# Optimization experiments

Hardware: AMD Instinct MI355X
Metric: run time of the kernel (lower is better)

Reference implementation:

```python
import jax, jax.numpy as jnp
import numpy as np

EMBED = 512
QDIM = 512
VDIM = 512
SRC = 4096
BSZ = 64


def setup_inputs() -> dict:
    key = jax.random.key(0)
    ks = jax.random.split(key, 6)
    query = jax.random.normal(ks[0], (BSZ, QDIM), dtype=jnp.float32)
    value = jax.random.normal(ks[1], (SRC, BSZ, VDIM), dtype=jnp.float32)
    key_padding_mask = jnp.zeros((SRC, BSZ), dtype=bool)
    # params: torch init uniform(-0.1, 0.1); b=0, g=sqrt(1/embed)
    Wq = jax.random.uniform(ks[2], (EMBED, QDIM), minval=-0.1, maxval=0.1, dtype=jnp.float32)
    Wv = jax.random.uniform(ks[3], (EMBED, VDIM), minval=-0.1, maxval=0.1, dtype=jnp.float32)
    v = jax.random.uniform(ks[4], (EMBED,), minval=-0.1, maxval=0.1, dtype=jnp.float32)
    b = jnp.zeros((EMBED,), dtype=jnp.float32)
    g = jnp.full((1,), np.sqrt(1.0 / EMBED), dtype=jnp.float32)
    return {"query": query, "value": value, "key_padding_mask": key_padding_mask,
            "Wq": Wq, "Wv": Wv, "v": v, "b": b, "g": g}


def reference(query, value, key_padding_mask, Wq, Wv, v, b, g):
    # projected_query: [1, bsz, embed]; key: [src, bsz, embed]
    pq = (query @ Wq.T)[None, :, :]
    key = jnp.einsum('sbv,ev->sbe', value, Wv)
    normed_v = g * v / jnp.linalg.norm(v)  # [embed]
    # attn_scores: [src, bsz]
    attn_scores = jnp.einsum('e,sbe->sb', normed_v, jnp.tanh(pq + key + b))
    attn_scores = jnp.where(key_padding_mask, -jnp.inf, attn_scores)
    attn_scores = jax.nn.softmax(attn_scores, axis=0)
    # context: [bsz, value_dim]
    context = jnp.einsum('sb,sbv->bv', attn_scores, value)
    return (context, attn_scores, attn_scores)
```

## Files before the change

kernel.cpp:

```cpp
#include <hip/hip_runtime.h>
#include <hip/hip_bf16.h>
#include <math.h>

typedef __bf16 bf16x8 __attribute__((ext_vector_type(8)));
typedef __bf16 bf16x4 __attribute__((ext_vector_type(4)));
typedef float  f32x4  __attribute__((ext_vector_type(4)));

#define SRC 4096
#define BSZ 64
#define EMB 512
#define LDA 520

__device__ __forceinline__ float fast_tanh(float x) {
  float ax = fabsf(x);
  float t  = __expf(-2.0f * ax);
  float r  = 1.0f - 2.0f * t / (1.0f + t);
  return copysignf(r, x);
}

__global__ void prep_nv(const float* __restrict__ v, const float* __restrict__ g,
                        float* __restrict__ nv) {
  __shared__ float red[256];
  int t = threadIdx.x;
  float a = v[t], b = v[t + 256];
  red[t] = a * a + b * b;
  __syncthreads();
  for (int o = 128; o > 0; o >>= 1) {
    if (t < o) red[t] += red[t + o];
    __syncthreads();
  }
  float scale = g[0] / sqrtf(red[0]);
  nv[t]       = a * scale;
  nv[t + 256] = b * scale;
}

__global__ void prep_pqb(const float* __restrict__ query, const float* __restrict__ Wq,
                         const float* __restrict__ bias, float* __restrict__ pqb) {
  __shared__ float q[EMB];
  int b = blockIdx.x, t = threadIdx.x;
  q[t]       = query[b * EMB + t];
  q[t + 256] = query[b * EMB + t + 256];
  __syncthreads();
  for (int e = t; e < EMB; e += 256) {
    const float* wr = Wq + (size_t)e * EMB;
    float acc = 0.f;
#pragma unroll 4
    for (int k = 0; k < EMB; k += 4) {
      float4 qv = *reinterpret_cast<const float4*>(&q[k]);
      float4 wv = *reinterpret_cast<const float4*>(&wr[k]);
      acc += qv.x * wv.x + qv.y * wv.y + qv.z * wv.z + qv.w * wv.w;
    }
    pqb[b * EMB + e] = acc + bias[e];
  }
}

__global__ void pack_wv(const float* __restrict__ Wv, __bf16* __restrict__ wvpk) {
  int tid  = blockIdx.x * 256 + threadIdx.x;
  int lane = tid & 63;
  int ks   = (tid >> 6) & 15;
  int nsub = tid >> 10;
  int e  = nsub * 16 + (lane & 15);
  int k0 = ks * 32 + (lane >> 4) * 8;
  const float* src = Wv + (size_t)e * EMB + k0;
  bf16x8 o;
#pragma unroll
  for (int j = 0; j < 8; ++j) o[j] = (__bf16)src[j];
  *reinterpret_cast<bf16x8*>(wvpk + (size_t)tid * 8) = o;
}

__global__ __launch_bounds__(256, 2)
void scores_kernel(const float* __restrict__ value, const float* __restrict__ pqb,
                   const float* __restrict__ nv, const __bf16* __restrict__ wvpk,
                   float* __restrict__ scoresT) {
  __shared__ __bf16 As[BSZ * LDA];
  __shared__ float red[4][BSZ];
  const int s = blockIdx.x;
  const int t = threadIdx.x;

  const float* src = value + (size_t)s * (BSZ * EMB);
#pragma unroll
  for (int i = 0; i < 32; ++i) {
    int e0 = (i * 256 + t) * 4;
    float4 vv = *reinterpret_cast<const float4*>(src + e0);
    int row = e0 >> 9;
    int col = e0 & 511;
    bf16x4 o;
    o[0] = (__bf16)vv.x; o[1] = (__bf16)vv.y; o[2] = (__bf16)vv.z; o[3] = (__bf16)vv.w;
    *reinterpret_cast<bf16x4*>(&As[row * LDA + col]) = o;
  }
  __syncthreads();

  const int w  = t >> 6;
  const int l  = t & 63;
  const int lr = l & 15;
  const int lk = l >> 4;

  float sc[16];
#pragma unroll
  for (int i = 0; i < 16; ++i) sc[i] = 0.f;

  for (int outer = 0; outer < 2; ++outer) {
    const int nbase = outer * 256 + w * 64;
    f32x4 acc[4][4];
#pragma unroll
    for (int m = 0; m < 4; ++m)
#pragma unroll
      for (int n = 0; n < 4; ++n)
#pragma unroll
        for (int r = 0; r < 4; ++r) acc[m][n][r] = 0.f;

#pragma unroll 2
    for (int ks = 0; ks < 16; ++ks) {
      bf16x8 a[4], bfr[4];
#pragma unroll
      for (int m = 0; m < 4; ++m)
        a[m] = *reinterpret_cast<const bf16x8*>(&As[(m * 16 + lr) * LDA + ks * 32 + lk * 8]);
#pragma unroll
      for (int n = 0; n < 4; ++n)
        bfr[n] = *reinterpret_cast<const bf16x8*>(
            wvpk + ((size_t)((((nbase >> 4) + n) * 16 + ks) * 64 + l)) * 8);
#pragma unroll
      for (int m = 0; m < 4; ++m)
#pragma unroll
        for (int n = 0; n < 4; ++n)
          acc[m][n] = __builtin_amdgcn_mfma_f32_16x16x32_bf16(a[m], bfr[n], acc[m][n], 0, 0, 0);
    }

#pragma unroll
    for (int n = 0; n < 4; ++n) {
      int col = nbase + n * 16 + lr;
      float nvc = nv[col];
#pragma unroll
      for (int m = 0; m < 4; ++m) {
#pragma unroll
        for (int r = 0; r < 4; ++r) {
          int brow = m * 16 + lk * 4 + r;
          float x = acc[m][n][r] + pqb[brow * EMB + col];
          sc[m * 4 + r] += nvc * fast_tanh(x);
        }
      }
    }
  }

#pragma unroll
  for (int i = 0; i < 16; ++i) {
    float vsum = sc[i];
#pragma unroll
    for (int off = 1; off < 16; off <<= 1) vsum += __shfl_xor(vsum, off, 64);
    if (lr == 0) red[w][(i >> 2) * 16 + lk * 4 + (i & 3)] = vsum;
  }
  __syncthreads();
  if (t < BSZ) {
    float total = red[0][t] + red[1][t] + red[2][t] + red[3][t];
    scoresT[(size_t)t * SRC + s] = total;
  }
}

__global__ void softmax_k(const float* __restrict__ scoresT, const unsigned char* __restrict__ mask,
                          float* __restrict__ pT, float* __restrict__ attn0,
                          float* __restrict__ attn1) {
  __shared__ float buf[SRC];
  __shared__ float red[256];
  int b = blockIdx.x, t = threadIdx.x;
  float mx = -1e30f;
  for (int s = t; s < SRC; s += 256) {
    float x = scoresT[(size_t)b * SRC + s];
    if (mask[(size_t)s * BSZ + b]) x = -1e30f;
    buf[s] = x;
    mx = fmaxf(mx, x);
  }
  red[t] = mx; __syncthreads();
  for (int o = 128; o > 0; o >>= 1) { if (t < o) red[t] = fmaxf(red[t], red[t + o]); __syncthreads(); }
  mx = red[0]; __syncthreads();
  float sum = 0.f;
  for (int s = t; s < SRC; s += 256) { float e = __expf(buf[s] - mx); buf[s] = e; sum += e; }
  red[t] = sum; __syncthreads();
  for (int o = 128; o > 0; o >>= 1) { if (t < o) red[t] += red[t + o]; __syncthreads(); }
  float inv = 1.0f / red[0];
  for (int s = t; s < SRC; s += 256) {
    float p = buf[s] * inv;
    pT[(size_t)b * SRC + s] = p;
    attn0[(size_t)s * BSZ + b] = p;
    attn1[(size_t)s * BSZ + b] = p;
  }
}

__global__ void ctx_partial(const float* __restrict__ value, const float* __restrict__ pT,
                            float* __restrict__ parts) {
  int blk = blockIdx.x;
  int c = blk >> 6;
  int b = blk & 63;
  int t = threadIdx.x;
  float2 acc = make_float2(0.f, 0.f);
#pragma unroll 4
  for (int i = 0; i < 128; ++i) {
    int s = c * 128 + i;
    float p = pT[(size_t)b * SRC + s];
    float2 vv = *reinterpret_cast<const float2*>(value + ((size_t)(s * BSZ + b)) * EMB + t * 2);
    acc.x += p * vv.x;
    acc.y += p * vv.y;
  }
  *reinterpret_cast<float2*>(parts + (size_t)blk * EMB + t * 2) = acc;
}

__global__ void ctx_reduce(const float* __restrict__ parts, float* __restrict__ out_ctx) {
  int idx = blockIdx.x * 256 + threadIdx.x;
  float acc = 0.f;
#pragma unroll
  for (int c = 0; c < 32; ++c) acc += parts[(size_t)c * (BSZ * EMB) + idx];
  out_ctx[idx] = acc;
}

extern "C" void kernel_launch(void* const* d_in, const int* in_sizes, int n_in,
                              void* d_out, int out_size, void* d_ws, size_t ws_size,
                              hipStream_t stream) {
  const float* query        = (const float*)d_in[0];
  const float* value        = (const float*)d_in[1];
  const unsigned char* mask = (const unsigned char*)d_in[2];
  const float* Wq           = (const float*)d_in[3];
  const float* Wv           = (const float*)d_in[4];
  const float* v            = (const float*)d_in[5];
  const float* bias         = (const float*)d_in[6];
  const float* g            = (const float*)d_in[7];

  float* out_ctx = (float*)d_out;
  float* attn0   = (float*)d_out + BSZ * EMB;
  float* attn1   = attn0 + SRC * BSZ;

  char* ws = (char*)d_ws;
  float*  nv      = (float*)(ws);
  float*  pqb     = (float*)(ws + 2048);
  __bf16* wvpk    = (__bf16*)(ws + 2048 + 131072);
  float*  scoresT = (float*)(ws + 2048 + 131072 + 524288);
  float*  pT      = scoresT + SRC * BSZ;
  float*  parts   = pT + SRC * BSZ;

  prep_nv<<<1, 256, 0, stream>>>(v, g, nv);
  prep_pqb<<<BSZ, 256, 0, stream>>>(query, Wq, bias, pqb);
  pack_wv<<<128, 256, 0, stream>>>(Wv, wvpk);
  scores_kernel<<<SRC, 256, 0, stream>>>(value, pqb, nv, wvpk, scoresT);
  softmax_k<<<BSZ, 256, 0, stream>>>(scoresT, mask, pT, attn0, attn1);
  ctx_partial<<<BSZ * 32, 256, 0, stream>>>(value, pT, parts);
  ctx_reduce<<<128, 256, 0, stream>>>(parts, out_ctx);
}
```

Before: 1.043 ms.

## Pipeline value staging in scores kernel with swizzled LDS and wider blocks

The scores kernel now runs 512 threads per block, one 64-column tile per warp, and stages value in four 128-wide K chunks. Each chunk is loaded into registers while the previous chunks feed MFMAs, through a double-buffered, XOR-swizzled LDS layout that replaces the padded full-row copy. This is meant to hide global load latency and cut LDS use so more blocks fit per CU, at the cost of extra barriers. Separately, prep_pqb is split across twice as many blocks with two accumulators, and ctx_partial switches to float4 loads with 128 threads.

```diff
diff --git a/kernel.cpp b/kernel.cpp
--- a/kernel.cpp
+++ b/kernel.cpp
@@ -9,7 +9,6 @@
 #define SRC 4096
 #define BSZ 64
 #define EMB 512
-#define LDA 520
 
 __device__ __forceinline__ float fast_tanh(float x) {
   float ax = fabsf(x);
@@ -37,21 +36,23 @@
 __global__ void prep_pqb(const float* __restrict__ query, const float* __restrict__ Wq,
                          const float* __restrict__ bias, float* __restrict__ pqb) {
   __shared__ float q[EMB];
-  int b = blockIdx.x, t = threadIdx.x;
+  int b = blockIdx.x >> 1, t = threadIdx.x;
+  int e = (blockIdx.x & 1) * 256 + t;
   q[t]       = query[b * EMB + t];
   q[t + 256] = query[b * EMB + t + 256];
   __syncthreads();
-  for (int e = t; e < EMB; e += 256) {
-    const float* wr = Wq + (size_t)e * EMB;
-    float acc = 0.f;
-#pragma unroll 4
-    for (int k = 0; k < EMB; k += 4) {
-      float4 qv = *reinterpret_cast<const float4*>(&q[k]);
-      float4 wv = *reinterpret_cast<const float4*>(&wr[k]);
-      acc += qv.x * wv.x + qv.y * wv.y + qv.z * wv.z + qv.w * wv.w;
-    }
-    pqb[b * EMB + e] = acc + bias[e];
-  }
+  const float* wr = Wq + (size_t)e * EMB;
+  float a0 = 0.f, a1 = 0.f;
+#pragma unroll 8
+  for (int k = 0; k < EMB; k += 8) {
+    float4 q0 = *reinterpret_cast<const float4*>(&q[k]);
+    float4 w0 = *reinterpret_cast<const float4*>(&wr[k]);
+    float4 q1 = *reinterpret_cast<const float4*>(&q[k + 4]);
+    float4 w1 = *reinterpret_cast<const float4*>(&wr[k + 4]);
+    a0 += q0.x * w0.x + q0.y * w0.y + q0.z * w0.z + q0.w * w0.w;
+    a1 += q1.x * w1.x + q1.y * w1.y + q1.z * w1.z + q1.w * w1.w;
+  }
+  pqb[b * EMB + e] = a0 + a1 + bias[e];
 }
 
 __global__ void pack_wv(const float* __restrict__ Wv, __bf16* __restrict__ wvpk) {
@@ -68,80 +69,104 @@
   *reinterpret_cast<bf16x8*>(wvpk + (size_t)tid * 8) = o;
 }
 
-__global__ __launch_bounds__(256, 2)
+__global__ __launch_bounds__(512, 4)
 void scores_kernel(const float* __restrict__ value, const float* __restrict__ pqb,
                    const float* __restrict__ nv, const __bf16* __restrict__ wvpk,
                    float* __restrict__ scoresT) {
-  __shared__ __bf16 As[BSZ * LDA];
-  __shared__ float red[4][BSZ];
+  __shared__ __bf16 As[2][64 * 128];
+  __shared__ float red[8][BSZ];
   const int s = blockIdx.x;
   const int t = threadIdx.x;
-
-  const float* src = value + (size_t)s * (BSZ * EMB);
-#pragma unroll
-  for (int i = 0; i < 32; ++i) {
-    int e0 = (i * 256 + t) * 4;
-    float4 vv = *reinterpret_cast<const float4*>(src + e0);
-    int row = e0 >> 9;
-    int col = e0 & 511;
-    bf16x4 o;
-    o[0] = (__bf16)vv.x; o[1] = (__bf16)vv.y; o[2] = (__bf16)vv.z; o[3] = (__bf16)vv.w;
-    *reinterpret_cast<bf16x4*>(&As[row * LDA + col]) = o;
-  }
-  __syncthreads();
-
   const int w  = t >> 6;
   const int l  = t & 63;
   const int lr = l & 15;
   const int lk = l >> 4;
 
-  float sc[16];
-#pragma unroll
-  for (int i = 0; i < 16; ++i) sc[i] = 0.f;
-
-  for (int outer = 0; outer < 2; ++outer) {
-    const int nbase = outer * 256 + w * 64;
-    f32x4 acc[4][4];
-#pragma unroll
-    for (int m = 0; m < 4; ++m)
-#pragma unroll
-      for (int n = 0; n < 4; ++n)
-#pragma unroll
-        for (int r = 0; r < 4; ++r) acc[m][n][r] = 0.f;
-
-#pragma unroll 2
-    for (int ks = 0; ks < 16; ++ks) {
-      bf16x8 a[4], bfr[4];
-#pragma unroll
-      for (int m = 0; m < 4; ++m)
-        a[m] = *reinterpret_cast<const bf16x8*>(&As[(m * 16 + lr) * LDA + ks * 32 + lk * 8]);
-#pragma unroll
-      for (int n = 0; n < 4; ++n)
-        bfr[n] = *reinterpret_cast<const bf16x8*>(
-            wvpk + ((size_t)((((nbase >> 4) + n) * 16 + ks) * 64 + l)) * 8);
-#pragma unroll
-      for (int m = 0; m < 4; ++m)
+  const int srow = t >> 3;
+  const int ssub = t & 7;
+  const float* sbase = value + (size_t)s * (BSZ * EMB) + (size_t)srow * EMB + ssub * 4;
+
+  float4 h0[4], h1[4];
+  auto issue = [&](int c, float4* h) {
+    const float* p = sbase + c * 128;
+#pragma unroll
+    for (int j = 0; j < 4; ++j) h[j] = *reinterpret_cast<const float4*>(p + j * 32);
+  };
+  auto write_lds = [&](int buf, const float4* h) {
+#pragma unroll
+    for (int j = 0; j < 4; ++j) {
+      int kg  = (ssub >> 1) + j * 4;
+      int kgp = kg ^ (srow & 7);
+      bf16x4 o;
+      o[0] = (__bf16)h[j].x; o[1] = (__bf16)h[j].y;
+      o[2] = (__bf16)h[j].z; o[3] = (__bf16)h[j].w;
+      *reinterpret_cast<bf16x4*>(&As[buf][srow * 128 + kgp * 8 + (ssub & 1) * 4]) = o;
+    }
+  };
+
+  f32x4 acc[4][4];
+#pragma unroll
+  for (int m = 0; m < 4; ++m)
+#pragma unroll
+    for (int n = 0; n < 4; ++n)
+#pragma unroll
+      for (int r = 0; r < 4; ++r) acc[m][n][r] = 0.f;
+
+  auto compute_chunk = [&](int buf, int c) {
+#pragma unroll
+    for (int ks = 0; ks < 4; ++ks) {
+      const int ksg = c * 4 + ks;
+      bf16x8 bq[4];
+#pragma unroll
+      for (int n = 0; n < 4; ++n) {
+        int nt = w * 4 + n;
+        bq[n] = *reinterpret_cast<const bf16x8*>(
+            wvpk + ((size_t)((nt * 16 + ksg) * 64 + l)) * 8);
+      }
+      const int kgp = ((ks * 4 + lk) ^ (lr & 7)) * 8;
+#pragma unroll
+      for (int m = 0; m < 4; ++m) {
+        bf16x8 a = *reinterpret_cast<const bf16x8*>(&As[buf][(m * 16 + lr) * 128 + kgp]);
 #pragma unroll
         for (int n = 0; n < 4; ++n)
-          acc[m][n] = __builtin_amdgcn_mfma_f32_16x16x32_bf16(a[m], bfr[n], acc[m][n], 0, 0, 0);
-    }
-
-#pragma unroll
-    for (int n = 0; n < 4; ++n) {
-      int col = nbase + n * 16 + lr;
-      float nvc = nv[col];
-#pragma unroll
-      for (int m = 0; m < 4; ++m) {
-#pragma unroll
-        for (int r = 0; r < 4; ++r) {
-          int brow = m * 16 + lk * 4 + r;
-          float x = acc[m][n][r] + pqb[brow * EMB + col];
-          sc[m * 4 + r] += nvc * fast_tanh(x);
-        }
+          acc[m][n] = __builtin_amdgcn_mfma_f32_16x16x32_bf16(a, bq[n], acc[m][n], 0, 0, 0);
       }
     }
-  }
-
+  };
+
+  issue(0, h0);
+  issue(1, h1);
+  write_lds(0, h0);
+  write_lds(1, h1);
+  __syncthreads();
+  issue(2, h0);
+  issue(3, h1);
+  compute_chunk(0, 0);
+  compute_chunk(1, 1);
+  __syncthreads();
+  write_lds(0, h0);
+  write_lds(1, h1);
+  __syncthreads();
+  compute_chunk(0, 2);
+  compute_chunk(1, 3);
+
+  float sc[16];
+#pragma unroll
+  for (int i = 0; i < 16; ++i) sc[i] = 0.f;
+#pragma unroll
+  for (int n = 0; n < 4; ++n) {
+    int col = w * 64 + n * 16 + lr;
+    float nvc = nv[col];
+#pragma unroll
+    for (int m = 0; m < 4; ++m) {
+#pragma unroll
+      for (int r = 0; r < 4; ++r) {
+        int brow = m * 16 + lk * 4 + r;
+        float x = acc[m][n][r] + pqb[brow * EMB + col];
+        sc[m * 4 + r] += nvc * fast_tanh(x);
+      }
+    }
+  }
 #pragma unroll
   for (int i = 0; i < 16; ++i) {
     float vsum = sc[i];
@@ -151,7 +176,9 @@
   }
   __syncthreads();
   if (t < BSZ) {
-    float total = red[0][t] + red[1][t] + red[2][t] + red[3][t];
+    float total = 0.f;
+#pragma unroll
+    for (int ww = 0; ww < 8; ++ww) total += red[ww][t];
     scoresT[(size_t)t * SRC + s] = total;
   }
 }
@@ -191,16 +218,16 @@
   int c = blk >> 6;
   int b = blk & 63;
   int t = threadIdx.x;
-  float2 acc = make_float2(0.f, 0.f);
-#pragma unroll 4
+  const float* pb = pT + (size_t)b * SRC + c * 128;
+  float4 acc = make_float4(0.f, 0.f, 0.f, 0.f);
+#pragma unroll 8
   for (int i = 0; i < 128; ++i) {
-    int s = c * 128 + i;
-    float p = pT[(size_t)b * SRC + s];
-    float2 vv = *reinterpret_cast<const float2*>(value + ((size_t)(s * BSZ + b)) * EMB + t * 2);
-    acc.x += p * vv.x;
-    acc.y += p * vv.y;
-  }
-  *reinterpret_cast<float2*>(parts + (size_t)blk * EMB + t * 2) = acc;
+    float p = pb[i];
+    float4 vv = *reinterpret_cast<const float4*>(
+        value + ((size_t)((c * 128 + i) * BSZ + b)) * EMB + t * 4);
+    acc.x += p * vv.x; acc.y += p * vv.y; acc.z += p * vv.z; acc.w += p * vv.w;
+  }
+  *reinterpret_cast<float4*>(parts + (size_t)blk * EMB + t * 4) = acc;
 }
 
 __global__ void ctx_reduce(const float* __restrict__ parts, float* __restrict__ out_ctx) {
@@ -236,10 +263,10 @@
   float*  parts   = pT + SRC * BSZ;
 
   prep_nv<<<1, 256, 0, stream>>>(v, g, nv);
-  prep_pqb<<<BSZ, 256, 0, stream>>>(query, Wq, bias, pqb);
+  prep_pqb<<<2 * BSZ, 256, 0, stream>>>(query, Wq, bias, pqb);
   pack_wv<<<128, 256, 0, stream>>>(Wv, wvpk);
-  scores_kernel<<<SRC, 256, 0, stream>>>(value, pqb, nv, wvpk, scoresT);
+  scores_kernel<<<SRC, 512, 0, stream>>>(value, pqb, nv, wvpk, scoresT);
   softmax_k<<<BSZ, 256, 0, stream>>>(scoresT, mask, pT, attn0, attn1);
-  ctx_partial<<<BSZ * 32, 256, 0, stream>>>(value, pT, parts);
+  ctx_partial<<<BSZ * 32, 128, 0, stream>>>(value, pT, parts);
   ctx_reduce<<<128, 256, 0, stream>>>(parts, out_ctx);
 }
```

Result: no change. 1.030 ms (-1.2%).
